# Optimization experiments

Measured on AMD Instinct MI355X. Metric: run time of the kernel, lower is better.

The kernel has to match this reference:

```python
import jax, jax.numpy as jnp
import numpy as np

B, S, E, H, W, L = 2048, 50, 256, 512, 256, 50  # batch, seq, emb, hidden, weight, answer_seq_len
V = 50 + 1  # input_size + 1 embedding rows


def _uni(k, shape, bound):
    return jax.random.uniform(k, shape, jnp.float32, -bound, bound)


def setup_inputs() -> dict:
    key = jax.random.key(0)
    ks = jax.random.split(key, 14)
    kb = 1.0 / np.sqrt(H)  # torch LSTM/Linear init bound 1/sqrt(hidden)
    inp = {
        'input': jax.random.randint(ks[0], (B, S), 0, V),
        'emb': jax.random.normal(ks[1], (V, E), jnp.float32),
        'enc_Wih': _uni(ks[2], (4 * H, E), kb),
        'enc_Whh': _uni(ks[3], (4 * H, H), kb),
        'enc_bih': _uni(ks[4], (4 * H,), kb),
        'enc_bhh': _uni(ks[5], (4 * H,), kb),
        'dec_Wih': _uni(ks[6], (4 * H, E), kb),
        'dec_Whh': _uni(ks[7], (4 * H, H), kb),
        'dec_bih': _uni(ks[8], (4 * H,), kb),
        'dec_bhh': _uni(ks[9], (4 * H,), kb),
        'W1': _uni(ks[10], (W, H), kb),
        'W2': _uni(ks[11], (W, H), kb),
        'vt': _uni(ks[12], (W,), 1.0 / np.sqrt(W)),
    }
    return inp


def _lstm_cell(x, h, c, Wih, Whh, bih, bhh):
    gates = x @ Wih.T + h @ Whh.T + (bih + bhh)
    i, f, g, o = jnp.split(gates, 4, axis=-1)  # torch gate order i,f,g,o
    c = jax.nn.sigmoid(f) * c + jax.nn.sigmoid(i) * jnp.tanh(g)
    h = jax.nn.sigmoid(o) * jnp.tanh(c)
    return h, c


def reference(input, emb, enc_Wih, enc_Whh, enc_bih, enc_bhh,
              dec_Wih, dec_Whh, dec_bih, dec_bhh, W1, W2, vt):
    x = emb[input]  # [B,S,E]

    def enc_step(carry, xt):
        h, c = carry
        h, c = _lstm_cell(xt, h, c, enc_Wih, enc_Whh, enc_bih, enc_bhh)
        return (h, c), h

    z = jnp.zeros((B, H), x.dtype)
    _, enc_seq = jax.lax.scan(enc_step, (z, z), x.transpose(1, 0, 2))  # [S,B,H]
    enc_states = enc_seq.transpose(1, 0, 2)  # [B,S,H]

    # W1(encoder_states) is loop-invariant; compute once (same math as per-step recompute)
    blend1 = jnp.einsum('bsh,wh->bsw', enc_states, W1)  # [B,S,W]

    dec_in = jnp.zeros((B, E), x.dtype)  # original never updates decoder_input
    h0 = jnp.zeros((B, H), x.dtype)
    c0 = enc_seq[-1]  # cell_state = encoder_states[-1]
    mask0 = jnp.zeros((B, S), bool)

    def dec_step(carry, k):
        h, c, mask = carry
        h, c = _lstm_cell(dec_in, h, c, dec_Wih, dec_Whh, dec_bih, dec_bhh)
        blend2 = h @ W2.T  # [B,W]
        scores = jnp.einsum('bsw,w->bs', jnp.tanh(blend1 + blend2[:, None, :]), vt)
        scores = jnp.where(mask, jnp.float32(-100000.0), scores)
        logp = jax.nn.log_softmax(scores, axis=-1)  # [B,S]
        chosen = jax.random.categorical(k, logp, axis=-1)  # [B]
        mask = mask.at[jnp.arange(B), chosen].set(True)
        return (h, c, mask), (logp, chosen)

    keys = jax.random.split(jax.random.key(42), L)
    _, (probs, tour) = jax.lax.scan(dec_step, (h0, c0, mask0), keys)
    probs = probs.transpose(1, 0, 2)  # [B,L,S]
    tour = tour.transpose(1, 0)       # [B,L]
    return probs, tour
```

## Files before the change

### kernel.cpp

```cpp
#include <hip/hip_runtime.h>
#include <cstdint>

#define Bsz 2048
#define Ssz 50
#define Esz 256
#define Hsz 512
#define Wsz 256
#define Lsz 50
#define Vsz 51
#define KI 16
#define CH 10
#define GFRAGC2 ((size_t)32 * 128 * 512)

#define JAX_THREEFRY_PARTITIONABLE 1

typedef _Float16 f16;
typedef _Float16 f16x8 __attribute__((ext_vector_type(8)));
typedef float f32x4 __attribute__((ext_vector_type(4)));

__host__ __device__ __forceinline__ void threefry2x32_hd(
    unsigned k0, unsigned k1, unsigned x0, unsigned x1,
    unsigned& o0, unsigned& o1) {
  unsigned ks2 = k0 ^ k1 ^ 0x1BD11BDAu;
  x0 += k0; x1 += k1;
#define TF_RND(r) { x0 += x1; x1 = (x1 << (r)) | (x1 >> (32 - (r))); x1 ^= x0; }
  TF_RND(13) TF_RND(15) TF_RND(26) TF_RND(6)
  x0 += k1; x1 += ks2 + 1u;
  TF_RND(17) TF_RND(29) TF_RND(16) TF_RND(24)
  x0 += ks2; x1 += k0 + 2u;
  TF_RND(13) TF_RND(15) TF_RND(26) TF_RND(6)
  x0 += k0; x1 += k1 + 3u;
  TF_RND(17) TF_RND(29) TF_RND(16) TF_RND(24)
  x0 += k1; x1 += ks2 + 4u;
  TF_RND(13) TF_RND(15) TF_RND(26) TF_RND(6)
  x0 += ks2; x1 += k0 + 5u;
#undef TF_RND
  o0 = x0; o1 = x1;
}

__global__ __launch_bounds__(512) void prep_gfrag(const float* __restrict__ Whh,
                                                  f16* __restrict__ dst) {
  int blk = blockIdx.x;
  int ntile = blk >> 5, kc = blk & 31;
  int t = threadIdx.x;
  int l = t >> 3, e = t & 7;
  int c = l & 15, kg = l >> 4;
  int n = ntile * 16 + c;
  int k = (kc & 15) * 32 + kg * 8 + e;
  int j = n >> 2, g = n & 3;
  float w = Whh[(size_t)(g * 512 + j) * 512 + k];
  f16 hi = (f16)w;
  float lo = w - (float)hi;
  f16 val = (kc < 16) ? hi : (f16)(lo * 2048.0f);
  dst[((size_t)kc * 128 + ntile) * 512 + t] = val;
}

__global__ __launch_bounds__(512) void prep_bfrag(const float* __restrict__ Wm,
                                                  f16* __restrict__ dst) {
  int blk = blockIdx.x;
  int wtile = blk >> 5, kc = blk & 31;
  int t = threadIdx.x;
  int l = t >> 3, e = t & 7;
  int c = l & 15, kg = l >> 4;
  int n = wtile * 16 + c;
  int k = (kc & 15) * 32 + kg * 8 + e;
  float w = Wm[(size_t)n * 512 + k];
  f16 hi = (f16)w;
  float lo = w - (float)hi;
  f16 val = (kc < 16) ? hi : (f16)(lo * 2048.0f);
  dst[((size_t)kc * 16 + wtile) * 512 + t] = val;
}

__global__ __launch_bounds__(256) void prep_encin(
    const float* __restrict__ emb, const float* __restrict__ Wih,
    const float* __restrict__ bih, const float* __restrict__ bhh,
    float* __restrict__ encInP) {
  int wid = blockIdx.x * 4 + (threadIdx.x >> 6);
  int lane = threadIdx.x & 63;
  if (wid >= Vsz * 2048) return;
  int v = wid >> 11, col = wid & 2047;
  float4 e = ((const float4*)emb)[v * 64 + lane];
  float4 w = ((const float4*)Wih)[col * 64 + lane];
  float d = e.x * w.x + e.y * w.y + e.z * w.z + e.w * w.w;
  for (int off = 32; off; off >>= 1) d += __shfl_xor(d, off);
  if (lane == 0) {
    int g = col >> 9, j = col & 511;
    encInP[(size_t)v * 2048 + j * 4 + g] = d + bih[col] + bhh[col];
  }
}

__global__ __launch_bounds__(256) void prep_dbias(const float* __restrict__ a,
                                                  const float* __restrict__ b,
                                                  float* __restrict__ dst) {
  int col = blockIdx.x * 256 + threadIdx.x;
  int g = col >> 9, j = col & 511;
  dst[j * 4 + g] = a[col] + b[col];
}

__global__ __launch_bounds__(256, 2) void gates_mfma(
    const f16* __restrict__ Afrag,
    const f16* __restrict__ Bfrag,
    const float* __restrict__ addtab, const int* __restrict__ input, int tstep,
    f16* __restrict__ Aout,
    float* __restrict__ cio) {
  __shared__ float Cst[64][132];
  const int t = threadIdx.x;
  const int lane = t & 63;
  const int wid = t >> 6;
  const int wm = wid >> 1, wn = wid & 1;
  const int bid = blockIdx.x;
  const int xcd = bid & 7, loc = bid >> 3;
  const int mblk = xcd * 4 + (loc >> 4);
  const int nblk = loc & 15;

  const f16* Ab = Afrag + (size_t)(mblk * 4 + wm * 2) * 512 + lane * 8;
  const f16* Bb = Bfrag + (size_t)(nblk * 8 + wn * 4) * 512 + lane * 8;

  f32x4 acc1[2][4], acc2[2][4];
  {
    f32x4 z = {0.f, 0.f, 0.f, 0.f};
#pragma unroll
    for (int i = 0; i < 2; ++i)
#pragma unroll
      for (int j = 0; j < 4; ++j) { acc1[i][j] = z; acc2[i][j] = z; }
  }

  f16x8 pah[2], pal[2], pbh[4], pbl[4];
  f16x8 qah[2], qal[2], qbh[4], qbl[4];

#define GLOAD(AH_, AL_, BH_, BL_, ki_)                                        \
  {                                                                           \
    const f16* ak = Ab + (size_t)(ki_)*65536;                                 \
    const f16* bk = Bb + (size_t)(ki_)*65536;                                 \
    _Pragma("unroll")                                                         \
    for (int q = 0; q < 2; ++q) {                                             \
      AH_[q] = *(const f16x8*)(ak + q * 512);                                 \
      AL_[q] = *(const f16x8*)(ak + (size_t)16 * 65536 + q * 512);            \
    }                                                                         \
    _Pragma("unroll")                                                         \
    for (int q = 0; q < 4; ++q) {                                             \
      BH_[q] = *(const f16x8*)(bk + q * 512);                                 \
      BL_[q] = *(const f16x8*)(bk + (size_t)16 * 65536 + q * 512);            \
    }                                                                         \
  }
#define GMM(AH_, AL_, BH_, BL_)                                               \
  {                                                                           \
    _Pragma("unroll")                                                         \
    for (int mt = 0; mt < 2; ++mt)                                            \
      _Pragma("unroll")                                                       \
      for (int nt = 0; nt < 4; ++nt)                                          \
        acc1[mt][nt] = __builtin_amdgcn_mfma_f32_16x16x32_f16(                \
            AH_[mt], BH_[nt], acc1[mt][nt], 0, 0, 0);                         \
    _Pragma("unroll")                                                         \
    for (int mt = 0; mt < 2; ++mt)                                            \
      _Pragma("unroll")                                                       \
      for (int nt = 0; nt < 4; ++nt)                                          \
        acc1[mt][nt] = __builtin_amdgcn_mfma_f32_16x16x32_f16(                \
            AL_[mt], BH_[nt], acc1[mt][nt], 0, 0, 0);                         \
    _Pragma("unroll")                                                         \
    for (int mt = 0; mt < 2; ++mt)                                            \
      _Pragma("unroll")                                                       \
      for (int nt = 0; nt < 4; ++nt)                                          \
        acc2[mt][nt] = __builtin_amdgcn_mfma_f32_16x16x32_f16(                \
            AH_[mt], BL_[nt], acc2[mt][nt], 0, 0, 0);                         \
  }

  GLOAD(pah, pal, pbh, pbl, 0)
#pragma unroll 1
  for (int ki = 0; ki < KI; ki += 2) {
    GLOAD(qah, qal, qbh, qbl, ki + 1)
    GMM(pah, pal, pbh, pbl)
    if (ki + 2 < KI) GLOAD(pah, pal, pbh, pbl, ki + 2)
    GMM(qah, qal, qbh, qbl)
  }
#undef GLOAD
#undef GMM

#pragma unroll
  for (int mt = 0; mt < 2; ++mt)
#pragma unroll
    for (int nt = 0; nt < 4; ++nt)
#pragma unroll
      for (int rg = 0; rg < 4; ++rg)
        Cst[wm * 32 + mt * 16 + (lane >> 4) * 4 + rg]
           [wn * 64 + nt * 16 + (lane & 15)] =
            acc1[mt][nt][rg] + acc2[mt][nt][rg] * (1.0f / 2048.0f);
  __syncthreads();

  const int bloc = t & 63, jg = t >> 6;
  const int bg = mblk * 64 + bloc;
  const float* arow = input
      ? addtab + (size_t)input[(size_t)bg * Ssz + tstep] * 2048
      : addtab;

  const int j0 = nblk * 32 + jg * 8;
  float* cp = cio + (size_t)bg * 512 + j0;
  float4 cv0 = *(const float4*)(cp);
  float4 cv1 = *(const float4*)(cp + 4);
  float cin[8] = {cv0.x, cv0.y, cv0.z, cv0.w, cv1.x, cv1.y, cv1.z, cv1.w};
  float cn[8], hv[8];
#pragma unroll
  for (int jj = 0; jj < 8; ++jj) {
    float4 gq = *(const float4*)(&Cst[bloc][jg * 32 + jj * 4]);
    float4 av = *(const float4*)(arow + (size_t)(j0 + jj) * 4);
    float gi = gq.x + av.x;
    float gf = gq.y + av.y;
    float gg = gq.z + av.z;
    float go = gq.w + av.w;
    float si = 1.0f / (1.0f + expf(-gi));
    float sf = 1.0f / (1.0f + expf(-gf));
    float sg = tanhf(gg);
    float so = 1.0f / (1.0f + expf(-go));
    float c2 = sf * cin[jj] + si * sg;
    cn[jj] = c2;
    hv[jj] = so * tanhf(c2);
  }
  *(float4*)(cp)     = make_float4(cn[0], cn[1], cn[2], cn[3]);
  *(float4*)(cp + 4) = make_float4(cn[4], cn[5], cn[6], cn[7]);

  f16x8 hi8, lo8;
#pragma unroll
  for (int jj = 0; jj < 8; ++jj) {
    f16 hi = (f16)hv[jj];
    hi8[jj] = hi;
    lo8[jj] = (f16)(hv[jj] - (float)hi);
  }
  const int kcH = j0 >> 5;
  const int kg = (j0 >> 3) & 3;
  size_t base = (((size_t)kcH * 128 + (bg >> 4)) * 64 + kg * 16 + (bg & 15)) * 8;
  *(f16x8*)(Aout + base)                       = hi8;
  *(f16x8*)(Aout + base + (size_t)16 * 65536)  = lo8;
}

__global__ __launch_bounds__(256) void blend_big(
    const f16* __restrict__ hChunk, const f16* __restrict__ Wb,
    float* __restrict__ outBase, int stepStride, int rowStride) {
  const int t = threadIdx.x, lane = t & 63, wid = t >> 6;
  const int wm = wid >> 1, wn = wid & 1;
  const int bid = blockIdx.x;
  const int xcd = bid & 7;
  const int r1 = bid >> 3;
  const int nblk = r1 & 7;
  const int r2 = r1 >> 3;
  const int mrem = r2 & 3;
  const int s = r2 >> 2;
  const int mblkL = xcd * 4 + mrem;
  const f16* Ab = hChunk + (size_t)s * GFRAGC2
                + (size_t)(mblkL * 4 + wm * 2) * 512 + lane * 8;
  const f16* Bb = Wb + (size_t)(nblk * 2 + wn) * 512 + lane * 8;

  f32x4 acc1[2], acc2[2];
  {
    f32x4 z = {0.f, 0.f, 0.f, 0.f};
    acc1[0] = z; acc1[1] = z; acc2[0] = z; acc2[1] = z;
  }
  f16x8 pah[2], pal[2], pbh, pbl, qah[2], qal[2], qbh, qbl;

#define BLOAD(AH_, AL_, BH_, BL_, ki_)                                        \
  {                                                                           \
    const f16* ak = Ab + (size_t)(ki_)*65536;                                 \
    const f16* bk = Bb + (size_t)(ki_)*8192;                                  \
    _Pragma("unroll")                                                         \
    for (int q = 0; q < 2; ++q) {                                             \
      AH_[q] = *(const f16x8*)(ak + q * 512);                                 \
      AL_[q] = *(const f16x8*)(ak + (size_t)16 * 65536 + q * 512);            \
    }                                                                         \
    BH_ = *(const f16x8*)(bk);                                                \
    BL_ = *(const f16x8*)(bk + (size_t)16 * 8192);                            \
  }
#define BMM(AH_, AL_, BH_, BL_)                                               \
  {                                                                           \
    _Pragma("unroll")                                                         \
    for (int mt = 0; mt < 2; ++mt)                                            \
      acc1[mt] = __builtin_amdgcn_mfma_f32_16x16x32_f16(                      \
          AH_[mt], BH_, acc1[mt], 0, 0, 0);                                   \
    _Pragma("unroll")                                                         \
    for (int mt = 0; mt < 2; ++mt)                                            \
      acc1[mt] = __builtin_amdgcn_mfma_f32_16x16x32_f16(                      \
          AL_[mt], BH_, acc1[mt], 0, 0, 0);                                   \
    _Pragma("unroll")                                                         \
    for (int mt = 0; mt < 2; ++mt)                                            \
      acc2[mt] = __builtin_amdgcn_mfma_f32_16x16x32_f16(                      \
          AH_[mt], BL_, acc2[mt], 0, 0, 0);                                   \
  }

  BLOAD(pah, pal, pbh, pbl, 0)
#pragma unroll 1
  for (int ki = 0; ki < KI; ki += 2) {
    BLOAD(qah, qal, qbh, qbl, ki + 1)
    BMM(pah, pal, pbh, pbl)
    if (ki + 2 < KI) BLOAD(pah, pal, pbh, pbl, ki + 2)
    BMM(qah, qal, qbh, qbl)
  }
#undef BLOAD
#undef BMM

  const int r = lane & 15, rg4 = (lane >> 4) * 4;
  float* ob = outBase + (size_t)s * stepStride;
#pragma unroll
  for (int mt = 0; mt < 2; ++mt)
#pragma unroll
    for (int rg = 0; rg < 4; ++rg) {
      int b = mblkL * 64 + wm * 32 + mt * 16 + rg4 + rg;
      int w = nblk * 32 + wn * 16 + r;
      ob[(size_t)b * rowStride + w] = acc1[mt][rg] + acc2[mt][rg] * (1.0f / 2048.0f);
    }
}

__global__ __launch_bounds__(256) void dec_cinit(const f16* __restrict__ hE,
                                                 float* __restrict__ cD) {
  int idx = blockIdx.x * 256 + threadIdx.x;
  int b = idx >> 9, j = idx & 511;
  size_t base = (((size_t)(j >> 5) * 128 + (b >> 4)) * 64
                 + ((j >> 3) & 3) * 16 + (b & 15)) * 8 + (j & 7);
  cD[idx] = (float)hE[base] + (float)hE[base + (size_t)16 * 65536];
}

__global__ __launch_bounds__(256) void sample_chunk(
    const float* __restrict__ b1, const float* __restrict__ b2c,
    const float* __restrict__ vt, unsigned long long* __restrict__ mask,
    float* __restrict__ probs, float* __restrict__ tour, int k0) {
  __shared__ float b1s[Ssz * Wsz];
  __shared__ float b2s[Wsz];
  __shared__ float vts[Wsz];
  __shared__ float sc[52];
  const int t = threadIdx.x, b = blockIdx.x;
  vts[t] = vt[t];
  {
    const float4* src = (const float4*)(b1 + (size_t)b * Ssz * Wsz);
    for (int i = t; i < (Ssz * Wsz) / 4; i += 256)
      ((float4*)b1s)[i] = src[i];
  }
  unsigned long long m = mask[b];
  const int wave = t >> 6, lane = t & 63;

  for (int kk = 0; kk < CH; ++kk) {
    const int stepk = k0 + kk;
    __syncthreads();
    b2s[t] = b2c[((size_t)kk * Bsz + b) * Wsz + t];
    __syncthreads();
    for (int s = wave; s < Ssz; s += 4) {
      const float* row = b1s + s * Wsz;
      float v = 0.f;
#pragma unroll
      for (int q = 0; q < 4; ++q) {
        int w = lane + 64 * q;
        v += vts[w] * tanhf(row[w] + b2s[w]);
      }
      for (int off = 32; off; off >>= 1) v += __shfl_xor(v, off);
      if (lane == 0) sc[s] = v;
    }
    __syncthreads();
    if (wave == 0) {
      float x = (lane < Ssz) ? sc[lane] : -INFINITY;
      if (lane < Ssz && ((m >> lane) & 1ull)) x = -100000.0f;
      float mv = x;
      for (int off = 32; off; off >>= 1) mv = fmaxf(mv, __shfl_xor(mv, off));
      float sh = x - mv;
      float e = (lane < Ssz) ? expf(sh) : 0.f;
      float ssum = e;
      for (int off = 32; off; off >>= 1) ssum += __shfl_xor(ssum, off);
      float lg = logf(ssum);
      float logp = sh - lg;
      if (lane < Ssz) probs[(size_t)b * (Lsz * Ssz) + stepk * Ssz + lane] = logp;

      unsigned kA, kB;
#if JAX_THREEFRY_PARTITIONABLE
      threefry2x32_hd(0u, 42u, 0u, (unsigned)stepk, kA, kB);
#else
      {
        unsigned a0, a1, c0, c1;
        int k = stepk;
        if (k < 25) {
          threefry2x32_hd(0u, 42u, 2u * k,      2u * k + 50u, a0, a1); kA = a0;
          threefry2x32_hd(0u, 42u, 2u * k + 1u, 2u * k + 51u, c0, c1); kB = c0;
        } else {
          threefry2x32_hd(0u, 42u, 2u * k - 50u, 2u * k,      a0, a1); kA = a1;
          threefry2x32_hd(0u, 42u, 2u * k - 49u, 2u * k + 1u, c0, c1); kB = c1;
        }
      }
#endif
      float val = -INFINITY;
      if (lane < Ssz) {
        unsigned j = (unsigned)(b * Ssz + lane);
        unsigned o0, o1, bits;
#if JAX_THREEFRY_PARTITIONABLE
        threefry2x32_hd(kA, kB, 0u, j, o0, o1);
        bits = o0 ^ o1;
#else
        if (j < 51200u) { threefry2x32_hd(kA, kB, j, j + 51200u, o0, o1); bits = o0; }
        else           { threefry2x32_hd(kA, kB, j - 51200u, j, o0, o1); bits = o1; }
#endif
        float f = __uint_as_float((bits >> 9) | 0x3F800000u) - 1.0f;
        float u = fmaxf(1.17549435e-38f, f + 1.17549435e-38f);
        val = logp - logf(-logf(u));
      }
      int idx = lane;
      for (int off = 32; off; off >>= 1) {
        float ov = __shfl_xor(val, off);
        int oi = __shfl_xor(idx, off);
        if (ov > val || (ov == val && oi < idx)) { val = ov; idx = oi; }
      }
      if (lane == 0) tour[(size_t)b * Lsz + stepk] = (float)idx;
      m |= (1ull << idx);
    }
  }
  if (t == 0) mask[b] = m;
}

extern "C" void kernel_launch(void* const* d_in, const int* in_sizes, int n_in,
                              void* d_out, int out_size, void* d_ws, size_t ws_size,
                              hipStream_t stream) {
  (void)in_sizes; (void)n_in; (void)out_size; (void)ws_size;
  const int*   input = (const int*)d_in[0];
  const float* emb   = (const float*)d_in[1];
  const float* eWih  = (const float*)d_in[2];
  const float* eWhh  = (const float*)d_in[3];
  const float* ebih  = (const float*)d_in[4];
  const float* ebhh  = (const float*)d_in[5];
  const float* dWhh  = (const float*)d_in[7];
  const float* dbih  = (const float*)d_in[8];
  const float* dbhh  = (const float*)d_in[9];
  const float* W1    = (const float*)d_in[10];
  const float* W2    = (const float*)d_in[11];
  const float* vt    = (const float*)d_in[12];
  float* outF = (float*)d_out;

  float* wsf = (float*)d_ws;
  size_t o = 0;
  const size_t BFRAG = (size_t)32 * 16 * 512;
  f16* BfE = (f16*)(wsf + o); o += GFRAGC2 / 2;
  f16* BfD = (f16*)(wsf + o); o += GFRAGC2 / 2;
  f16* Bb1 = (f16*)(wsf + o); o += BFRAG / 2;
  f16* Bb2 = (f16*)(wsf + o); o += BFRAG / 2;
  float* encInP = wsf + o; o += (size_t)Vsz * 2048;
  float* dbiasP = wsf + o; o += 2048;
  f16* hZero = (f16*)(wsf + o); o += GFRAGC2 / 2;
  f16* hBuf  = (f16*)(wsf + o); o += CH * (GFRAGC2 / 2);
  float* cE  = wsf + o; o += (size_t)Bsz * Hsz;
  float* b2c = wsf + o; o += (size_t)CH * Bsz * Wsz;
  float* b1  = wsf + o; o += (size_t)Bsz * Ssz * Wsz;
  unsigned long long* maskp = (unsigned long long*)(wsf + o); o += Bsz * 2;

  hipMemsetAsync(hZero, 0, GFRAGC2 * 2, stream);
  hipMemsetAsync(cE, 0, (size_t)Bsz * Hsz * 4, stream);
  hipMemsetAsync(maskp, 0, (size_t)Bsz * 8, stream);

  prep_gfrag<<<128 * 32, 512, 0, stream>>>(eWhh, BfE);
  prep_gfrag<<<128 * 32, 512, 0, stream>>>(dWhh, BfD);
  prep_bfrag<<<16 * 32, 512, 0, stream>>>(W1, Bb1);
  prep_bfrag<<<16 * 32, 512, 0, stream>>>(W2, Bb2);
  prep_encin<<<(Vsz * 2048) / 4, 256, 0, stream>>>(emb, eWih, ebih, ebhh, encInP);
  prep_dbias<<<8, 256, 0, stream>>>(dbih, dbhh, dbiasP);

  const size_t GF = GFRAGC2;

  for (int c = 0; c < Ssz / CH; ++c) {
    for (int s = 0; s < CH; ++s) {
      int t = c * CH + s;
      const f16* in = (t == 0) ? hZero : hBuf + (size_t)((t - 1) % CH) * GF;
      gates_mfma<<<512, 256, 0, stream>>>(in, BfE, encInP, input, t,
                                          hBuf + (size_t)s * GF, cE);
    }
    blend_big<<<8 * 8 * 4 * CH, 256, 0, stream>>>(hBuf, Bb1,
                                                  b1 + (size_t)(c * CH) * Wsz,
                                                  Wsz, Ssz * Wsz);
  }
  dec_cinit<<<(Bsz * Hsz) / 256, 256, 0, stream>>>(
      hBuf + (size_t)((Ssz - 1) % CH) * GF, cE);

  for (int c = 0; c < Lsz / CH; ++c) {
    for (int s = 0; s < CH; ++s) {
      int k = c * CH + s;
      const f16* in = (k == 0) ? hZero : hBuf + (size_t)((k - 1) % CH) * GF;
      gates_mfma<<<512, 256, 0, stream>>>(in, BfD, dbiasP, nullptr, 0,
                                          hBuf + (size_t)s * GF, cE);
    }
    blend_big<<<8 * 8 * 4 * CH, 256, 0, stream>>>(hBuf, Bb2, b2c,
                                                  Bsz * Wsz, Wsz);
    sample_chunk<<<Bsz, 256, 0, stream>>>(b1, b2c, vt, maskp, outF,
                                          outF + (size_t)Bsz * Lsz * Ssz,
                                          c * CH);
  }
}
```

Measured before the change: 3.940 ms.

## Overlap score computation with sampling via warp specialization and fast tanh

Rewrites sample_chunk to use 512 threads, with seven waves computing attention scores for the next step into a double-buffered shared array while the eighth wave runs softmax and sampling for the current step. vt and b2 are held in registers instead of shared memory, and tanhf is replaced with an exp-based fast approximation. The aim is to hide the serial sampling latency and cut synchronisation and transcendental cost. The fast tanh lowers accuracy and could flip sampled indices near ties.

```diff
diff --git a/kernel.cpp b/kernel.cpp
--- a/kernel.cpp
+++ b/kernel.cpp
@@ -38,6 +38,11 @@
   o0 = x0; o1 = x1;
 }
 
+__device__ __forceinline__ float tanh_fast(float x) {
+  float e = __expf(2.0f * x);
+  return 1.0f - __fdividef(2.0f, e + 1.0f);
+}
+
 __global__ __launch_bounds__(512) void prep_gfrag(const float* __restrict__ Whh,
                                                   f16* __restrict__ dst) {
   int blk = blockIdx.x;
@@ -316,42 +321,50 @@
   cD[idx] = (float)hE[base] + (float)hE[base + (size_t)16 * 65536];
 }
 
-__global__ __launch_bounds__(256) void sample_chunk(
+__global__ __launch_bounds__(512) void sample_chunk(
     const float* __restrict__ b1, const float* __restrict__ b2c,
     const float* __restrict__ vt, unsigned long long* __restrict__ mask,
     float* __restrict__ probs, float* __restrict__ tour, int k0) {
   __shared__ float b1s[Ssz * Wsz];
-  __shared__ float b2s[Wsz];
-  __shared__ float vts[Wsz];
-  __shared__ float sc[52];
+  __shared__ float scbuf[2][52];
   const int t = threadIdx.x, b = blockIdx.x;
-  vts[t] = vt[t];
+  const int wid = t >> 6, lane = t & 63;
   {
     const float4* src = (const float4*)(b1 + (size_t)b * Ssz * Wsz);
-    for (int i = t; i < (Ssz * Wsz) / 4; i += 256)
+    for (int i = t; i < (Ssz * Wsz) / 4; i += 512)
       ((float4*)b1s)[i] = src[i];
   }
-  unsigned long long m = mask[b];
-  const int wave = t >> 6, lane = t & 63;
-
+  const float vtr0 = vt[lane], vtr1 = vt[lane + 64];
+  const float vtr2 = vt[lane + 128], vtr3 = vt[lane + 192];
+  unsigned long long m = (wid == 7) ? mask[b] : 0ull;
+  __syncthreads();
+
+#define SCORE_ROWS(step_, dst_)                                               \
+  {                                                                           \
+    const float* b2p = b2c + ((size_t)(step_) * Bsz + b) * Wsz;               \
+    float b20 = b2p[lane], b21 = b2p[lane + 64];                              \
+    float b22 = b2p[lane + 128], b23 = b2p[lane + 192];                       \
+    for (int s = wid; s < Ssz; s += 7) {                                      \
+      const float* row = b1s + s * Wsz;                                       \
+      float v = vtr0 * tanh_fast(row[lane] + b20);                            \
+      v += vtr1 * tanh_fast(row[lane + 64] + b21);                            \
+      v += vtr2 * tanh_fast(row[lane + 128] + b22);                           \
+      v += vtr3 * tanh_fast(row[lane + 192] + b23);                           \
+      for (int off = 32; off; off >>= 1) v += __shfl_xor(v, off);             \
+      if (lane == 0) (dst_)[s] = v;                                           \
+    }                                                                         \
+  }
+
+  if (wid < 7) SCORE_ROWS(0, scbuf[0])
+  __syncthreads();
+
+#pragma unroll 1
   for (int kk = 0; kk < CH; ++kk) {
-    const int stepk = k0 + kk;
-    __syncthreads();
-    b2s[t] = b2c[((size_t)kk * Bsz + b) * Wsz + t];
-    __syncthreads();
-    for (int s = wave; s < Ssz; s += 4) {
-      const float* row = b1s + s * Wsz;
-      float v = 0.f;
-#pragma unroll
-      for (int q = 0; q < 4; ++q) {
-        int w = lane + 64 * q;
-        v += vts[w] * tanhf(row[w] + b2s[w]);
-      }
-      for (int off = 32; off; off >>= 1) v += __shfl_xor(v, off);
-      if (lane == 0) sc[s] = v;
-    }
-    __syncthreads();
-    if (wave == 0) {
+    if (wid < 7) {
+      if (kk + 1 < CH) SCORE_ROWS(kk + 1, scbuf[(kk + 1) & 1])
+    } else {
+      const float* sc = scbuf[kk & 1];
+      const int stepk = k0 + kk;
       float x = (lane < Ssz) ? sc[lane] : -INFINITY;
       if (lane < Ssz && ((m >> lane) & 1ull)) x = -100000.0f;
       float mv = x;
@@ -404,8 +417,10 @@
       if (lane == 0) tour[(size_t)b * Lsz + stepk] = (float)idx;
       m |= (1ull << idx);
     }
-  }
-  if (t == 0) mask[b] = m;
+    __syncthreads();
+  }
+#undef SCORE_ROWS
+  if (wid == 7 && lane == 0) mask[b] = m;
 }
 
 extern "C" void kernel_launch(void* const* d_in, const int* in_sizes, int n_in,
@@ -478,7 +493,7 @@
     }
     blend_big<<<8 * 8 * 4 * CH, 256, 0, stream>>>(hBuf, Bb2, b2c,
                                                   Bsz * Wsz, Wsz);
-    sample_chunk<<<Bsz, 256, 0, stream>>>(b1, b2c, vt, maskp, outF,
+    sample_chunk<<<Bsz, 512, 0, stream>>>(b1, b2c, vt, maskp, outF,
                                           outF + (size_t)Bsz * Lsz * Ssz,
                                           c * CH);
   }
```

Result: faster. 3.464 ms (-12.1%).
